# Kernel optimization log

Hardware: AMD Instinct MI355X
Metric: run time of the kernel (lower is better)

Reference implementation:

```python
import jax, jax.numpy as jnp
import numpy as np

D_MODEL = 512
N_HEADS = 8
D_K = D_MODEL // N_HEADS
MAX_LEN = 512  # max_seq_len; rel table has 2*MAX_LEN-1 rows


def setup_inputs() -> dict:
    key = jax.random.key(0)
    ks = jax.random.split(key, 7)
    B, S = 8, 512
    s = 1.0 / np.sqrt(D_MODEL)
    return {
        "x": jax.random.normal(ks[0], (B, S, D_MODEL), jnp.float32),
        "Wq": jax.random.normal(ks[1], (D_MODEL, D_MODEL), jnp.float32) * s,
        "bq": jnp.zeros((D_MODEL,), jnp.float32),
        "Wk": jax.random.normal(ks[2], (D_MODEL, D_MODEL), jnp.float32) * s,
        "bk": jnp.zeros((D_MODEL,), jnp.float32),
        "Wv": jax.random.normal(ks[3], (D_MODEL, D_MODEL), jnp.float32) * s,
        "bv": jnp.zeros((D_MODEL,), jnp.float32),
        "Wo": jax.random.normal(ks[4], (D_MODEL, D_MODEL), jnp.float32) * s,
        "bo": jnp.zeros((D_MODEL,), jnp.float32),
        "rel_embed": jax.random.normal(ks[5], (2 * MAX_LEN - 1, D_MODEL), jnp.float32) * 0.02,
    }


def reference(x, Wq, bq, Wk, bk, Wv, bv, Wo, bo, rel_embed):
    B, S, _ = x.shape
    scale = np.sqrt(D_K).astype(np.float32)

    def split_heads(t):  # (B,S,D) -> (B,H,S,dk)
        return t.reshape(B, S, N_HEADS, D_K).transpose(0, 2, 1, 3)

    q = split_heads(x @ Wq.T + bq)
    k = split_heads(x @ Wk.T + bk)
    v = split_heads(x @ Wv.T + bv)

    scores = jnp.einsum('bhqd,bhkd->bhqk', q, k) / scale

    # relative position bias: idx[q_pos, k_pos] = k_pos - q_pos + MAX_LEN - 1
    pos = jnp.arange(S)
    rel_idx = pos[None, :] - pos[:, None] + (MAX_LEN - 1)  # (S,S)
    rel_bias = rel_embed[rel_idx].reshape(S, S, N_HEADS, D_K)  # (S,S,H,dk)
    scores = scores + jnp.einsum('bhqd,qkhd->bhqk', q, rel_bias)

    attn = jax.nn.softmax(scores, axis=-1)
    out = jnp.einsum('bhqk,bhkd->bhqd', attn, v)  # (B,H,S,dk)
    out = out.transpose(0, 2, 1, 3).reshape(B, S, D_MODEL)
    return out @ Wo.T + bo
```

## Files before the change

kernel.cpp:

```cpp
#include <hip/hip_runtime.h>
#include <math.h>

#define B_  8
#define S_  512
#define D_  512
#define H_  8
#define DK_ 64

typedef __attribute__((ext_vector_type(8))) short short8;
typedef __attribute__((ext_vector_type(4))) float f32x4;

#define MFMA_BF16(a, b, c) __builtin_amdgcn_mfma_f32_16x16x32_bf16(a, b, c, 0, 0, 0)

__device__ __forceinline__ unsigned bf16_rne(float x) {
    unsigned u = __float_as_uint(x);
    return (u + 0x7FFFu + ((u >> 16) & 1u)) >> 16;
}
__device__ __forceinline__ float bf16f(unsigned h) { return __uint_as_float(h << 16); }

__device__ __forceinline__ void glds16(const ushort* g, ushort* l) {
    __builtin_amdgcn_global_load_lds(
        (const __attribute__((address_space(1))) unsigned int*)g,
        (__attribute__((address_space(3))) unsigned int*)l,
        16, 0, 0);
}

__global__ __launch_bounds__(256)
void conv_pl(const float* __restrict__ x,
             const float* __restrict__ wq, const float* __restrict__ wk,
             const float* __restrict__ wv, const float* __restrict__ wo,
             ushort* __restrict__ Xh, ushort* __restrict__ Xl,
             ushort* __restrict__ Wqh, ushort* __restrict__ Wql,
             ushort* __restrict__ Wkh, ushort* __restrict__ Wkl,
             ushort* __restrict__ Wvh, ushort* __restrict__ Wvl,
             ushort* __restrict__ Woh, ushort* __restrict__ Wol) {
    const int bid = blockIdx.x;
    const float* src; ushort* dh; ushort* dl; int i4;
    if (bid < 2048) {
        src = x; dh = Xh; dl = Xl; i4 = bid * 256 + threadIdx.x;
    } else {
        const int r = bid - 2048;
        const int wsel = r >> 8;
        src = (wsel == 0) ? wq : (wsel == 1) ? wk : (wsel == 2) ? wv : wo;
        dh  = (wsel == 0) ? Wqh : (wsel == 1) ? Wkh : (wsel == 2) ? Wvh : Woh;
        dl  = (wsel == 0) ? Wql : (wsel == 1) ? Wkl : (wsel == 2) ? Wvl : Wol;
        i4 = (r & 255) * 256 + threadIdx.x;
    }
    const float4 v = ((const float4*)src)[i4];
    unsigned h[4], l[4];
    const float* vp = &v.x;
    #pragma unroll
    for (int j = 0; j < 4; ++j) { h[j] = bf16_rne(vp[j]); l[j] = bf16_rne(vp[j] - bf16f(h[j])); }
    ((uint2*)dh)[i4] = make_uint2(h[0] | (h[1] << 16), h[2] | (h[3] << 16));
    ((uint2*)dl)[i4] = make_uint2(l[0] | (l[1] << 16), l[2] | (l[3] << 16));
}

__global__ __launch_bounds__(256)
void conv_rel(const float* __restrict__ rel, ushort* __restrict__ Rg) {
    const int idx = blockIdx.x * 256 + threadIdx.x;
    const int d2 = idx & 31;
    const int rr = (idx >> 5) % 1152;
    const int h  = idx / (1152 * 32);
    unsigned v0 = 0, v1 = 0;
    if (rr >= 64 && rr < 64 + 1023) {
        const float* s = &rel[(size_t)(rr - 64) * 512 + h * 64 + d2 * 2];
        v0 = bf16_rne(s[0]); v1 = bf16_rne(s[1]);
    }
    *(uint*)&Rg[((size_t)h * 1152 + rr) * 64 + d2 * 2] = v0 | (v1 << 16);
}

template<int XB, int OM>
__global__ __launch_bounds__(256, 2)
void gemm_mfma(const ushort* __restrict__ Xhp, const ushort* __restrict__ Xlp,
               const ushort* __restrict__ Yh0, const ushort* __restrict__ Yl0,
               const ushort* __restrict__ Yh1, const ushort* __restrict__ Yl1,
               const float* __restrict__ bias0, const float* __restrict__ bias1,
               float scale0, float scale1,
               float* __restrict__ outF,
               ushort* __restrict__ oh0, ushort* __restrict__ ol0,
               ushort* __restrict__ oh1, ushort* __restrict__ ol1) {
    __shared__ ushort Xs[2][2][64 * 64];
    __shared__ ushort Ys[2][2][64 * 64];

    const int z = blockIdx.z;
    const ushort* Yhp = z ? Yh1 : Yh0;
    const ushort* Ylp = z ? Yl1 : Yl0;
    const float*  bias = z ? bias1 : bias0;
    const float   scale = z ? scale1 : scale0;
    ushort* ohp = z ? oh1 : oh0;
    ushort* olp = z ? ol1 : ol0;

    const int tid = threadIdx.x;
    const int w = tid >> 6, lane = tid & 63;
    const int g = lane >> 4, c = lane & 15;
    const int rloc = lane >> 3, cc8 = lane & 7;
    const int cp = cc8 ^ rloc;
    const int r0 = blockIdx.y * 64;
    const int c0 = blockIdx.x * 64;

    const f32x4 fz = {0.f, 0.f, 0.f, 0.f};
    f32x4 acc[2][2] = {{fz, fz}, {fz, fz}};

    auto stage = [&](int kt, int buf) {
        const int k0 = kt * 64;
        const ushort* gb; ushort* lb; size_t rstr;
        if (w < 2) {
            const ushort* Xp = (w == 1) ? Xlp : Xhp;
            if (XB == 0) { gb = Xp + (size_t)r0 * 512 + k0; rstr = 512; }
            else {
                const int b = r0 >> 9, s0 = r0 & 511, h = k0 >> 6;
                gb = Xp + (((size_t)(b * 8 + h)) * 512 + s0) * 64; rstr = 64;
            }
            lb = &Xs[buf][w][0];
        } else {
            gb = ((w == 2) ? Yhp : Ylp) + (size_t)c0 * 512 + k0; rstr = 512;
            lb = &Ys[buf][w - 2][0];
        }
        #pragma unroll
        for (int j = 0; j < 8; ++j)
            glds16(gb + (size_t)(j * 8 + rloc) * rstr + cp * 8, lb + j * 512);
    };

    auto compute = [&](int buf) {
        #pragma unroll
        for (int ks = 0; ks < 2; ++ks) {
            short8 axh[2], axl[2], byh[2], byl[2];
            const int wm = (w >> 1) * 32, wn = (w & 1) * 32;
            #pragma unroll
            for (int t = 0; t < 2; ++t) {
                int row = wm + t * 16 + c;
                int off = row * 64 + (((ks * 4 + g) ^ (row & 7)) * 8);
                axh[t] = *(const short8*)&Xs[buf][0][off];
                axl[t] = *(const short8*)&Xs[buf][1][off];
                row = wn + t * 16 + c;
                off = row * 64 + (((ks * 4 + g) ^ (row & 7)) * 8);
                byh[t] = *(const short8*)&Ys[buf][0][off];
                byl[t] = *(const short8*)&Ys[buf][1][off];
            }
            #pragma unroll
            for (int tm = 0; tm < 2; ++tm)
                #pragma unroll
                for (int tn = 0; tn < 2; ++tn) {
                    acc[tm][tn] = MFMA_BF16(axh[tm], byh[tn], acc[tm][tn]);
                    acc[tm][tn] = MFMA_BF16(axl[tm], byh[tn], acc[tm][tn]);
                    acc[tm][tn] = MFMA_BF16(axh[tm], byl[tn], acc[tm][tn]);
                }
        }
    };

    stage(0, 0);
    __syncthreads();
    for (int kt = 0; kt < 8; ++kt) {
        if (kt < 7) stage(kt + 1, (kt + 1) & 1);
        compute(kt & 1);
        __syncthreads();
    }

    const int wm = (w >> 1) * 32, wn = (w & 1) * 32;
    if (OM == 0) {
        #pragma unroll
        for (int tn = 0; tn < 2; ++tn) {
            const int gc = c0 + wn + tn * 16 + c;
            const float bv = bias[gc];
            #pragma unroll
            for (int tm = 0; tm < 2; ++tm)
                #pragma unroll
                for (int i = 0; i < 4; ++i) {
                    const int gr = r0 + wm + tm * 16 + g * 4 + i;
                    outF[(size_t)gr * 512 + gc] = acc[tm][tn][i] + bv;
                }
        }
    } else if (OM == 2) {
        #pragma unroll
        for (int tn = 0; tn < 2; ++tn) {
            const int gc = c0 + wn + tn * 16 + c;
            const int h = gc >> 6, dk = gc & 63;
            const float bv = bias[gc];
            #pragma unroll
            for (int tm = 0; tm < 2; ++tm)
                #pragma unroll
                for (int i = 0; i < 4; ++i) {
                    const int gr = r0 + wm + tm * 16 + g * 4 + i;
                    const int b = gr >> 9, s = gr & 511;
                    const float v = (acc[tm][tn][i] + bv) * scale;
                    const unsigned hb = bf16_rne(v);
                    const size_t a = (((size_t)(b * 8 + h)) * 512 + s) * 64 + dk;
                    ohp[a] = (ushort)hb;
                    olp[a] = (ushort)bf16_rne(v - bf16f(hb));
                }
        }
    } else {
        #pragma unroll
        for (int tm = 0; tm < 2; ++tm)
            #pragma unroll
            for (int i = 0; i < 4; ++i) {
                const int gr = r0 + wm + tm * 16 + g * 4 + i;
                const int h = gr >> 6, dk = gr & 63;
                const float bv = bias[gr];
                #pragma unroll
                for (int tn = 0; tn < 2; ++tn) {
                    const int gc = c0 + wn + tn * 16 + c;
                    const int b = gc >> 9, s = gc & 511;
                    const float v = acc[tm][tn][i] + bv;
                    const size_t a = (((size_t)(b * 8 + h)) * 64 + dk) * 512 + s;
                    ohp[a] = (ushort)bf16_rne(v);
                }
            }
    }
}

__global__ __launch_bounds__(256, 2)
void attn_mfma(const ushort* __restrict__ Qhp, const ushort* __restrict__ Qlp,
               const ushort* __restrict__ Khp, const ushort* __restrict__ Klp,
               const ushort* __restrict__ Vhp, const ushort* __restrict__ Rg,
               float* __restrict__ Op0, float* __restrict__ Op1,
               float2* __restrict__ Ml0, float2* __restrict__ Ml1) {
    __shared__ ushort Ksm[2][64 * 64];
    __shared__ ushort Vsm[64 * 64];
    __shared__ ushort Rsm[128 * 64];
    __shared__ ushort Usm[4][16 * 86];

    const int tid  = threadIdx.x;
    const int w    = tid >> 6;
    const int lane = tid & 63;
    const int g    = lane >> 4;
    const int c    = lane & 15;
    const int rloc = lane >> 3, cc8 = lane & 7;
    const int bh   = blockIdx.y;
    const int h    = bh & 7;
    const int z    = blockIdx.z;
    const int qwb  = blockIdx.x * 64;
    const int qw   = qwb + w * 16;

    float* __restrict__ Op = z ? Op1 : Op0;
    float2* __restrict__ Ml = z ? Ml1 : Ml0;

    short8 qfh[2], qfl[2];
    #pragma unroll
    for (int ks = 0; ks < 2; ++ks) {
        const size_t qi = ((size_t)bh * 512 + qw + c) * 64 + ks * 32 + g * 8;
        qfh[ks] = *(const short8*)&Qhp[qi];
        qfl[ks] = *(const short8*)&Qlp[qi];
    }

    const f32x4 fz = {0.f, 0.f, 0.f, 0.f};
    f32x4 o[4] = {fz, fz, fz, fz};
    float m = -INFINITY, l = 0.f;

    const ushort* KhB = Khp + (size_t)bh * 512 * 64;
    const ushort* KlB = Klp + (size_t)bh * 512 * 64;
    const ushort* VhB = Vhp + (size_t)bh * 64 * 512;
    const ushort* RgH = Rg + (size_t)h * 1152 * 64;

    for (int kt = z * 4; kt < z * 4 + 4; ++kt) {
        const int k0 = kt * 64;
        const int rbase = k0 - qwb + 512;
        __syncthreads();

        #pragma unroll
        for (int j = 0; j < 4; ++j) {
            const int cd  = j * 256 + tid;
            const int row = cd >> 3, cc = cd & 7;
            const uint4 v = *(const uint4*)&RgH[(size_t)(rbase + row) * 64 + cc * 8];
            *(uint4*)&Rsm[row * 64 + ((cc ^ (row & 7)) << 3)] = v;
        }

        if (w < 2) {
            const ushort* gb = (w == 0) ? KhB : KlB;
            ushort* lb = &Ksm[w][0];
            #pragma unroll
            for (int j = 0; j < 8; ++j) {
                const int row = j * 8 + rloc;
                const int tcq = row >> 4, cq = row & 15;
                const int key = ((tcq & 1) << 5) + ((cq >> 2) << 3)
                              + ((tcq >> 1) << 2) + (cq & 3);
                glds16(gb + (size_t)(k0 + key) * 64 + ((cc8 ^ rloc) << 3),
                       lb + j * 512);
            }
        } else {
            const ushort* gb = VhB + k0 + (size_t)(w - 2) * 32 * 512;
            ushort* lb = &Vsm[(w - 2) * 32 * 64];
            #pragma unroll
            for (int j = 0; j < 4; ++j)
                glds16(gb + (size_t)(j * 8 + rloc) * 512 + ((cc8 ^ rloc) << 3),
                       lb + j * 512);
        }
        __syncthreads();

        f32x4 u[5];
        #pragma unroll
        for (int ut = 0; ut < 5; ++ut) u[ut] = fz;
        #pragma unroll
        for (int ks = 0; ks < 2; ++ks)
            #pragma unroll
            for (int ut = 0; ut < 5; ++ut) {
                const int rl = 48 - 16 * w + c + ut * 16;
                const short8 rf = *(const short8*)
                    &Rsm[rl * 64 + (((ks * 4 + g) ^ (c & 7)) << 3)];
                u[ut] = MFMA_BF16(qfh[ks], rf, u[ut]);
            }
        #pragma unroll
        for (int ut = 0; ut < 5; ++ut)
            #pragma unroll
            for (int i = 0; i < 4; ++i)
                Usm[w][(g * 4 + i) * 86 + c + ut * 16] = (ushort)bf16_rne(u[ut][i]);

        f32x4 st[4];
        #pragma unroll
        for (int tc = 0; tc < 4; ++tc) st[tc] = fz;
        #pragma unroll
        for (int ks = 0; ks < 2; ++ks)
            #pragma unroll
            for (int tc = 0; tc < 4; ++tc) {
                const int row = tc * 16 + c;
                const int chv = ((ks * 4 + g) ^ (row & 7)) * 8;
                const short8 kh8 = *(const short8*)&Ksm[0][row * 64 + chv];
                const short8 kl8 = *(const short8*)&Ksm[1][row * 64 + chv];
                st[tc] = MFMA_BF16(kh8, qfh[ks], st[tc]);
                st[tc] = MFMA_BF16(kh8, qfl[ks], st[tc]);
                st[tc] = MFMA_BF16(kl8, qfh[ks], st[tc]);
            }

        asm volatile("s_waitcnt lgkmcnt(0)" ::: "memory");

        #pragma unroll
        for (int tc = 0; tc < 4; ++tc)
            #pragma unroll
            for (int i = 0; i < 4; ++i) {
                const int key = ((tc & 1) << 5) + 8 * g + ((tc >> 1) << 2) + i;
                st[tc][i] += bf16f(Usm[w][c * 85 + key + 15]);
            }

        float tm = fmaxf(fmaxf(st[0][0], st[0][1]), fmaxf(st[0][2], st[0][3]));
        #pragma unroll
        for (int tc = 1; tc < 4; ++tc) {
            const float t2 = fmaxf(fmaxf(st[tc][0], st[tc][1]),
                                   fmaxf(st[tc][2], st[tc][3]));
            tm = fmaxf(tm, t2);
        }
        tm = fmaxf(tm, __shfl_xor(tm, 16));
        tm = fmaxf(tm, __shfl_xor(tm, 32));
        const float mn = fmaxf(m, tm);
        const float corr = __expf(m - mn);
        m = mn;
        l *= corr;
        #pragma unroll
        for (int dt = 0; dt < 4; ++dt) o[dt] *= corr;

        uint pk[4][2];
        #pragma unroll
        for (int tc = 0; tc < 4; ++tc) {
            const float p0 = __expf(st[tc][0] - mn);
            const float p1 = __expf(st[tc][1] - mn);
            const float p2 = __expf(st[tc][2] - mn);
            const float p3 = __expf(st[tc][3] - mn);
            l += (p0 + p1) + (p2 + p3);
            pk[tc][0] = bf16_rne(p0) | (bf16_rne(p1) << 16);
            pk[tc][1] = bf16_rne(p2) | (bf16_rne(p3) << 16);
        }

        #pragma unroll
        for (int ks = 0; ks < 2; ++ks) {
            union { uint u4[4]; short8 s8; } pb;
            pb.u4[0] = pk[ks][0];
            pb.u4[1] = pk[ks][1];
            pb.u4[2] = pk[ks + 2][0];
            pb.u4[3] = pk[ks + 2][1];
            #pragma unroll
            for (int dt = 0; dt < 4; ++dt) {
                const int row = dt * 16 + c;
                const int chv = ((ks * 4 + g) ^ (row & 7)) * 8;
                const short8 vh8 = *(const short8*)&Vsm[row * 64 + chv];
                o[dt] = MFMA_BF16(vh8, pb.s8, o[dt]);
            }
        }
    }

    float lt = l;
    lt += __shfl_xor(lt, 16);
    lt += __shfl_xor(lt, 32);
    if (lane < 16) Ml[(size_t)bh * 512 + qw + c] = make_float2(m, lt);
    #pragma unroll
    for (int dt = 0; dt < 4; ++dt)
        #pragma unroll
        for (int i = 0; i < 4; ++i)
            Op[((size_t)bh * 64 + dt * 16 + g * 4 + i) * 512 + qw + c] = o[dt][i];
}

__global__ __launch_bounds__(256)
void attn_combine(const float* __restrict__ Op0, const float* __restrict__ Op1,
                  const float2* __restrict__ Ml0, const float2* __restrict__ Ml1,
                  ushort* __restrict__ Oh, ushort* __restrict__ Ol) {
    __shared__ float L0[64][67];
    __shared__ float L1[64][67];
    const int t = threadIdx.x;
    const int bh = blockIdx.y;
    const int s0 = blockIdx.x * 64;
    #pragma unroll
    for (int j = 0; j < 4; ++j) {
        const int d = (t >> 4) + j * 16;
        const int c4 = (t & 15) * 4;
        const size_t ga = ((size_t)bh * 64 + d) * 512 + s0 + c4;
        *(float4*)&L0[d][c4] = *(const float4*)&Op0[ga];
        *(float4*)&L1[d][c4] = *(const float4*)&Op1[ga];
    }
    __syncthreads();
    const int sl = t >> 2;
    const int d0 = (t & 3) * 16;
    const float2 a = Ml0[(size_t)bh * 512 + s0 + sl];
    const float2 b = Ml1[(size_t)bh * 512 + s0 + sl];
    const float mm = fmaxf(a.x, b.x);
    float w0 = __expf(a.x - mm), w1 = __expf(b.x - mm);
    const float inv = 1.0f / (a.y * w0 + b.y * w1);
    w0 *= inv; w1 *= inv;
    const size_t ob = ((size_t)bh * 512 + s0 + sl) * 64 + d0;
    #pragma unroll
    for (int q = 0; q < 4; ++q) {
        unsigned hb[4], lb4[4];
        #pragma unroll
        for (int e = 0; e < 4; ++e) {
            const int dd = q * 4 + e;
            const float v = L0[d0 + dd][sl] * w0 + L1[d0 + dd][sl] * w1;
            hb[e] = bf16_rne(v);
            lb4[e] = bf16_rne(v - bf16f(hb[e]));
        }
        *(uint2*)&Oh[ob + q * 4] = make_uint2(hb[0] | (hb[1] << 16), hb[2] | (hb[3] << 16));
        *(uint2*)&Ol[ob + q * 4] = make_uint2(lb4[0] | (lb4[1] << 16), lb4[2] | (lb4[3] << 16));
    }
}

extern "C" void kernel_launch(void* const* d_in, const int* in_sizes, int n_in,
                              void* d_out, int out_size, void* d_ws, size_t ws_size,
                              hipStream_t stream) {
    const float* x   = (const float*)d_in[0];
    const float* Wq  = (const float*)d_in[1];
    const float* bq  = (const float*)d_in[2];
    const float* Wk  = (const float*)d_in[3];
    const float* bk  = (const float*)d_in[4];
    const float* Wv  = (const float*)d_in[5];
    const float* bv  = (const float*)d_in[6];
    const float* Wo  = (const float*)d_in[7];
    const float* bo  = (const float*)d_in[8];
    const float* rel = (const float*)d_in[9];
    float* out = (float*)d_out;

    const size_t NP = (size_t)B_ * H_ * S_ * DK_;
    const size_t WP = (size_t)D_ * D_;
    ushort* Xh  = (ushort*)d_ws;
    ushort* Xl  = Xh + NP;
    ushort* Wqh = Xl + NP;
    ushort* Wql = Wqh + WP;
    ushort* Wkh = Wql + WP;
    ushort* Wkl = Wkh + WP;
    ushort* Wvh = Wkl + WP;
    ushort* Wvl = Wvh + WP;
    ushort* Woh = Wvl + WP;
    ushort* Wol = Woh + WP;
    ushort* Qh  = Wol + WP;
    ushort* Ql  = Qh + NP;
    ushort* Kh  = Ql + NP;
    ushort* Kl  = Kh + NP;
    ushort* Vh  = Kl + NP;
    ushort* Rg  = Vh + NP;
    float*  Op1 = (float*)(Rg + 589824);
    float2* Ml0 = (float2*)(Op1 + NP);
    float2* Ml1 = Ml0 + 32768;
    float*  Op0 = (float*)d_ws;

    conv_pl<<<3072, 256, 0, stream>>>(x, Wq, Wk, Wv, Wo,
                                      Xh, Xl, Wqh, Wql, Wkh, Wkl, Wvh, Wvl, Woh, Wol);
    conv_rel<<<1152, 256, 0, stream>>>(rel, Rg);

    gemm_mfma<0, 2><<<dim3(8, 64, 2), 256, 0, stream>>>(
        Xh, Xl, Wqh, Wql, Wkh, Wkl, bq, bk, 1.0f, 0.125f,
        nullptr, Qh, Ql, Kh, Kl);
    gemm_mfma<0, 3><<<dim3(64, 8, 1), 256, 0, stream>>>(
        Wvh, Wvl, Xh, Xl, nullptr, nullptr, bv, nullptr, 1.0f, 1.0f,
        nullptr, Vh, nullptr, nullptr, nullptr);

    attn_mfma<<<dim3(8, 64, 2), 256, 0, stream>>>(
        Qh, Ql, Kh, Kl, Vh, Rg, Op0, Op1, Ml0, Ml1);

    attn_combine<<<dim3(8, 64), 256, 0, stream>>>(Op0, Op1, Ml0, Ml1, Kh, Kl);

    gemm_mfma<1, 0><<<dim3(8, 64, 1), 256, 0, stream>>>(
        Kh, Kl, Woh, Wol, nullptr, nullptr, bo, nullptr, 1.0f, 1.0f,
        out, nullptr, nullptr, nullptr, nullptr);
}
```

Baseline: 94.25 us.

## Register-prefetch next K/V/R tiles and alias U scratch into Rsm

Replaces the direct global-to-LDS loads with register prefetch: the next tile's K, V and relative-embedding rows are loaded into registers while the current tile is computed, then written to LDS at the top of the next iteration. The U scratch buffer is now aliased onto the Rsm region after an extra barrier, which shrinks LDS use, and launch bounds are raised to 4 blocks per CU to get more occupancy. The 10 uint4 prefetch registers and the tighter register budget may cause spills, and the added barrier adds a synchronisation point per tile.

Result: slower. 132.6 us (+40.7%).

```diff
diff --git a/kernel.cpp b/kernel.cpp
--- a/kernel.cpp
+++ b/kernel.cpp
@@ -209,7 +209,7 @@
     }
 }
 
-__global__ __launch_bounds__(256, 2)
+__global__ __launch_bounds__(256, 4)
 void attn_mfma(const ushort* __restrict__ Qhp, const ushort* __restrict__ Qlp,
                const ushort* __restrict__ Khp, const ushort* __restrict__ Klp,
                const ushort* __restrict__ Vhp, const ushort* __restrict__ Rg,
@@ -218,24 +218,77 @@
     __shared__ ushort Ksm[2][64 * 64];
     __shared__ ushort Vsm[64 * 64];
     __shared__ ushort Rsm[128 * 64];
-    __shared__ ushort Usm[4][16 * 86];
 
     const int tid  = threadIdx.x;
     const int w    = tid >> 6;
     const int lane = tid & 63;
     const int g    = lane >> 4;
     const int c    = lane & 15;
-    const int rloc = lane >> 3, cc8 = lane & 7;
     const int bh   = blockIdx.y;
     const int h    = bh & 7;
     const int z    = blockIdx.z;
     const int qwb  = blockIdx.x * 64;
     const int qw   = qwb + w * 16;
 
+    ushort* Usm = &Rsm[w * 1376];
+
     float* __restrict__ Op = z ? Op1 : Op0;
     float2* __restrict__ Ml = z ? Ml1 : Ml0;
 
+    const ushort* KhB = Khp + (size_t)bh * 512 * 64;
+    const ushort* KlB = Klp + (size_t)bh * 512 * 64;
+    const ushort* VhB = Vhp + (size_t)bh * 64 * 512;
+    const ushort* RgH = Rg + (size_t)h * 1152 * 64;
+
+    uint4 rv[10];
+    auto issue = [&](int kt) {
+        const int k0 = kt * 64;
+        const int rbase = k0 - qwb + 512;
+        #pragma unroll
+        for (int j = 0; j < 10; ++j) {
+            const int cd = j * 256 + tid;
+            const ushort* src;
+            if (j < 2) {
+                const int c2 = cd;
+                src = &KhB[(size_t)(k0 + (c2 >> 3)) * 64 + (c2 & 7) * 8];
+            } else if (j < 4) {
+                const int c2 = cd - 512;
+                src = &KlB[(size_t)(k0 + (c2 >> 3)) * 64 + (c2 & 7) * 8];
+            } else if (j < 6) {
+                const int c2 = cd - 1024;
+                src = &VhB[(size_t)(c2 >> 3) * 512 + k0 + (c2 & 7) * 8];
+            } else {
+                const int c2 = cd - 1536;
+                src = &RgH[(size_t)(rbase + (c2 >> 3)) * 64 + (c2 & 7) * 8];
+            }
+            rv[j] = *(const uint4*)src;
+        }
+    };
+    auto commit = [&]() {
+        #pragma unroll
+        for (int j = 0; j < 10; ++j) {
+            const int cd = j * 256 + tid;
+            if (j < 4) {
+                const int p = j >> 1;
+                const int c2 = cd & 511;
+                const int krow = c2 >> 3, cc = c2 & 7;
+                const int lrow = ((krow & 32) >> 1) | ((krow & 4) << 3)
+                               | ((krow & 24) >> 1) | (krow & 3);
+                *(uint4*)&Ksm[p][lrow * 64 + ((cc ^ (lrow & 7)) << 3)] = rv[j];
+            } else if (j < 6) {
+                const int c2 = cd - 1024;
+                const int row = c2 >> 3, cc = c2 & 7;
+                *(uint4*)&Vsm[row * 64 + ((cc ^ (row & 7)) << 3)] = rv[j];
+            } else {
+                const int c2 = cd - 1536;
+                const int row = c2 >> 3, cc = c2 & 7;
+                *(uint4*)&Rsm[row * 64 + ((cc ^ (row & 7)) << 3)] = rv[j];
+            }
+        }
+    };
+
     short8 qfh[2], qfl[2];
+    issue(z * 4);
     #pragma unroll
     for (int ks = 0; ks < 2; ++ks) {
         const size_t qi = ((size_t)bh * 512 + qw + c) * 64 + ks * 32 + g * 8;
@@ -247,44 +300,10 @@
     f32x4 o[4] = {fz, fz, fz, fz};
     float m = -INFINITY, l = 0.f;
 
-    const ushort* KhB = Khp + (size_t)bh * 512 * 64;
-    const ushort* KlB = Klp + (size_t)bh * 512 * 64;
-    const ushort* VhB = Vhp + (size_t)bh * 64 * 512;
-    const ushort* RgH = Rg + (size_t)h * 1152 * 64;
-
     for (int kt = z * 4; kt < z * 4 + 4; ++kt) {
-        const int k0 = kt * 64;
-        const int rbase = k0 - qwb + 512;
         __syncthreads();
-
-        #pragma unroll
-        for (int j = 0; j < 4; ++j) {
-            const int cd  = j * 256 + tid;
-            const int row = cd >> 3, cc = cd & 7;
-            const uint4 v = *(const uint4*)&RgH[(size_t)(rbase + row) * 64 + cc * 8];
-            *(uint4*)&Rsm[row * 64 + ((cc ^ (row & 7)) << 3)] = v;
-        }
-
-        if (w < 2) {
-            const ushort* gb = (w == 0) ? KhB : KlB;
-            ushort* lb = &Ksm[w][0];
-            #pragma unroll
-            for (int j = 0; j < 8; ++j) {
-                const int row = j * 8 + rloc;
-                const int tcq = row >> 4, cq = row & 15;
-                const int key = ((tcq & 1) << 5) + ((cq >> 2) << 3)
-                              + ((tcq >> 1) << 2) + (cq & 3);
-                glds16(gb + (size_t)(k0 + key) * 64 + ((cc8 ^ rloc) << 3),
-                       lb + j * 512);
-            }
-        } else {
-            const ushort* gb = VhB + k0 + (size_t)(w - 2) * 32 * 512;
-            ushort* lb = &Vsm[(w - 2) * 32 * 64];
-            #pragma unroll
-            for (int j = 0; j < 4; ++j)
-                glds16(gb + (size_t)(j * 8 + rloc) * 512 + ((cc8 ^ rloc) << 3),
-                       lb + j * 512);
-        }
+        commit();
+        if (kt + 1 < z * 4 + 4) issue(kt + 1);
         __syncthreads();
 
         f32x4 u[5];
@@ -299,11 +318,6 @@
                     &Rsm[rl * 64 + (((ks * 4 + g) ^ (c & 7)) << 3)];
                 u[ut] = MFMA_BF16(qfh[ks], rf, u[ut]);
             }
-        #pragma unroll
-        for (int ut = 0; ut < 5; ++ut)
-            #pragma unroll
-            for (int i = 0; i < 4; ++i)
-                Usm[w][(g * 4 + i) * 86 + c + ut * 16] = (ushort)bf16_rne(u[ut][i]);
 
         f32x4 st[4];
         #pragma unroll
@@ -321,6 +335,14 @@
                 st[tc] = MFMA_BF16(kl8, qfh[ks], st[tc]);
             }
 
+        __syncthreads();
+
+        #pragma unroll
+        for (int ut = 0; ut < 5; ++ut)
+            #pragma unroll
+            for (int i = 0; i < 4; ++i)
+                Usm[(g * 4 + i) * 86 + c + ut * 16] = (ushort)bf16_rne(u[ut][i]);
+
         asm volatile("s_waitcnt lgkmcnt(0)" ::: "memory");
 
         #pragma unroll
@@ -328,7 +350,7 @@
             #pragma unroll
             for (int i = 0; i < 4; ++i) {
                 const int key = ((tc & 1) << 5) + 8 * g + ((tc >> 1) << 2) + i;
-                st[tc][i] += bf16f(Usm[w][c * 85 + key + 15]);
+                st[tc][i] += bf16f(Usm[c * 85 + key + 15]);
             }
 
         float tm = fmaxf(fmaxf(st[0][0], st[0][1]), fmaxf(st[0][2], st[0][3]));
```
